# Kernel tuning notes

Measured on AMD Instinct MI355X. Metric: run time of the kernel, lower is better.

The kernel has to match this reference:

```python
import jax, jax.numpy as jnp
import numpy as np

B, N, H = 16384, 4, 768
HEADS, OUT = 4, H // 4
L = 3  # num_layers
NEG_SLOPE = 0.2
EPS = 1e-5


def layer_norm(x, g, b):
    m = jnp.mean(x, axis=-1, keepdims=True)
    v = jnp.mean((x - m) ** 2, axis=-1, keepdims=True)
    return (x - m) * jax.lax.rsqrt(v + EPS) * g + b


def setup_inputs() -> dict:
    key = jax.random.key(0)
    ks = jax.random.split(key, 12)
    s = 0.02
    return {
        "image_features": jax.random.normal(ks[0], (B, N, H), jnp.float32),
        "type_emb": s * jax.random.normal(ks[1], (N, H), jnp.float32),
        "W_gat": s * jax.random.normal(ks[2], (L, H, HEADS * OUT), jnp.float32),
        "att_src": s * jax.random.normal(ks[3], (L, HEADS, OUT), jnp.float32),
        "att_dst": s * jax.random.normal(ks[4], (L, HEADS, OUT), jnp.float32),
        "gat_bias": jnp.zeros((L, H), jnp.float32),
        "ln_gamma": jnp.ones((L, H), jnp.float32),
        "ln_beta": jnp.zeros((L, H), jnp.float32),
        "W1": s * jax.random.normal(ks[5], (L, H, 2 * H), jnp.float32),
        "b1": jnp.zeros((L, 2 * H), jnp.float32),
        "W2": s * jax.random.normal(ks[6], (L, 2 * H, H), jnp.float32),
        "b2": jnp.zeros((L, H), jnp.float32),
    }


def reference(image_features, type_emb, W_gat, att_src, att_dst, gat_bias,
              ln_gamma, ln_beta, W1, b1, W2, b2):
    # type embedding added per node type (N=4 fixed types)
    x = image_features + type_emb  # [B, N, H]
    for l in range(L):
        res = x
        # GATConv: fully-connected 4-node graph == dense per-head attention
        h = (x @ W_gat[l]).reshape(B, N, HEADS, OUT)          # [B, N, heads, out]
        a_s = jnp.einsum('bnhd,hd->bnh', h, att_src[l])        # alpha for source j
        a_d = jnp.einsum('bnhd,hd->bnh', h, att_dst[l])        # alpha for dest   i
        e = a_d[:, :, None, :] + a_s[:, None, :, :]            # [B, i, j, heads]
        e = jnp.where(e > 0, e, NEG_SLOPE * e)                 # leaky_relu(0.2)
        alpha = jax.nn.softmax(e, axis=2)                      # softmax over neighbors j
        out = jnp.einsum('bijh,bjhd->bihd', alpha, h).reshape(B, N, H) + gat_bias[l]
        x = layer_norm(out + res, ln_gamma[l], ln_beta[l])
        # FFN (dropout inactive at eval)
        ffn = jax.nn.relu(x @ W1[l] + b1[l]) @ W2[l] + b2[l]
        # NOTE: original module reuses the SAME LayerNorm for both residuals
        x = layer_norm(ffn + x, ln_gamma[l], ln_beta[l])
    return x
```

## Files before the change

kernel.cpp:

```cpp
#include <hip/hip_runtime.h>
#include <stdint.h>


typedef __bf16 bf16x8 __attribute__((ext_vector_type(8)));
typedef float  f32x4  __attribute__((ext_vector_type(4)));

__device__ __forceinline__ uint16_t f2bf(float f) {
  union { float f; uint32_t u; } v; v.f = f;
  uint32_t r = v.u + 0x7fffu + ((v.u >> 16) & 1u);
  return (uint16_t)(r >> 16);
}

__device__ __forceinline__ float wave_sum(float v) {
#pragma unroll
  for (int off = 32; off > 0; off >>= 1) v += __shfl_xor(v, off);
  return v;
}

__device__ __forceinline__ void gload_lds16(const void* g, void* l) {
  __builtin_amdgcn_global_load_lds(
      (const __attribute__((address_space(1))) void*)(g),
      (__attribute__((address_space(3))) void*)(l), 16, 0, 0);
}

template <int EPI>
__global__ __launch_bounds__(256, 2)
void gemm_bf16(const uint16_t* __restrict__ A, const uint16_t* __restrict__ Bt,
               const float* __restrict__ bias, void* __restrict__ Cv,
               int M, int N, int K) {
  __shared__ uint16_t As[128 * 32];
  __shared__ uint16_t Bs[128 * 32];

  int wgid = blockIdx.y * gridDim.x + blockIdx.x;
  const int nwg = gridDim.x * gridDim.y;
  if ((nwg & 7) == 0) wgid = (wgid & 7) * (nwg >> 3) + (wgid >> 3);
  const int bn = wgid % gridDim.x, bm = wgid / gridDim.x;

  const int t = threadIdx.x;
  const int w = t >> 6, lane = t & 63;
  const int wr = w >> 1, wc = w & 1;

  f32x4 acc[4][4] = {};

  const int srow = t >> 2;
  const int scol = (t & 3) * 8;
  const uint16_t* Ag = A  + (size_t)(bm * 128 + srow) * K + scol;
  const uint16_t* Bg = Bt + (size_t)(bn * 128 + srow) * K + scol;

  const int KT = K >> 5;
  for (int kt = 0; kt < KT; ++kt) {
    __syncthreads();
    gload_lds16(Ag,          &As[w * 512]);
    gload_lds16(Ag + 64 * K, &As[2048 + w * 512]);
    gload_lds16(Bg,          &Bs[w * 512]);
    gload_lds16(Bg + 64 * K, &Bs[2048 + w * 512]);
    Ag += 32; Bg += 32;
    asm volatile("s_waitcnt vmcnt(0)" ::: "memory");
    __syncthreads();

    const int fr = lane & 15;
    const int kg = (lane >> 4) * 8;
    bf16x8 a[4], b[4];
#pragma unroll
    for (int m = 0; m < 4; ++m)
      a[m] = *(const bf16x8*)&As[(wr * 64 + m * 16 + fr) * 32 + kg];
#pragma unroll
    for (int n = 0; n < 4; ++n)
      b[n] = *(const bf16x8*)&Bs[(wc * 64 + n * 16 + fr) * 32 + kg];
#pragma unroll
    for (int m = 0; m < 4; ++m)
#pragma unroll
      for (int n = 0; n < 4; ++n)
        acc[m][n] = __builtin_amdgcn_mfma_f32_16x16x32_bf16(a[m], b[n], acc[m][n], 0, 0, 0);
  }

  const int row0 = bm * 128 + wr * 64 + ((lane >> 4) * 4);
  const int col0 = bn * 128 + wc * 64 + (lane & 15);
#pragma unroll
  for (int m = 0; m < 4; ++m) {
#pragma unroll
    for (int n = 0; n < 4; ++n) {
      const int col = col0 + n * 16;
      const float bv = bias ? bias[col] : 0.0f;
#pragma unroll
      for (int j = 0; j < 4; ++j) {
        const int row = row0 + m * 16 + j;
        const float v = acc[m][n][j] + bv;
        if (EPI == 0) ((float*)Cv)[(size_t)row * N + col] = v;
        else ((uint16_t*)Cv)[(size_t)row * N + col] = f2bf(fmaxf(v, 0.0f));
      }
    }
  }
}

__global__ __launch_bounds__(256)
void transpose_f32_to_bf16(const float* __restrict__ W, uint16_t* __restrict__ Wt,
                           int R, int C) {
  __shared__ float tile[32][33];
  const size_t lofs = (size_t)blockIdx.z * R * C;
  W += lofs; Wt += lofs;
  const int c0 = blockIdx.x * 32, r0 = blockIdx.y * 32;
  const int t = threadIdx.x, tc = t & 31, tr = t >> 5;
#pragma unroll
  for (int i = 0; i < 4; ++i)
    tile[tr + i * 8][tc] = W[(size_t)(r0 + tr + i * 8) * C + c0 + tc];
  __syncthreads();
#pragma unroll
  for (int i = 0; i < 4; ++i)
    Wt[(size_t)(c0 + tr + i * 8) * R + r0 + tc] = f2bf(tile[tc][tr + i * 8]);
}

__global__ __launch_bounds__(256)
void init_x(const float* __restrict__ img, const float* __restrict__ te,
            float* __restrict__ xout, uint16_t* __restrict__ xb, int n4) {
  for (int i = blockIdx.x * 256 + threadIdx.x; i < n4; i += gridDim.x * 256) {
    const float4 a = ((const float4*)img)[i];
    const float4 b = ((const float4*)te)[i % 768];
    float4 o; o.x = a.x + b.x; o.y = a.y + b.y; o.z = a.z + b.z; o.w = a.w + b.w;
    ((float4*)xout)[i] = o;
    ushort4 p; p.x = f2bf(o.x); p.y = f2bf(o.y); p.z = f2bf(o.z); p.w = f2bf(o.w);
    ((ushort4*)xb)[i] = p;
  }
}

__global__ __launch_bounds__(256, 4)
void gat_attn_ln(const float* __restrict__ h, const float* __restrict__ xres,
                 const float* __restrict__ att_src, const float* __restrict__ att_dst,
                 const float* __restrict__ gbias, const float* __restrict__ gamma,
                 const float* __restrict__ beta, float* __restrict__ xout,
                 uint16_t* __restrict__ xb) {
  __shared__ float hs[4 * 768];
  __shared__ float as_[4][4], ad_[4][4];
  __shared__ float alpha[4][4][4];
  const int b = blockIdx.x;
  const int t = threadIdx.x, w = t >> 6, lane = t & 63;
  const size_t base = (size_t)b * 3072;

  {
    const float4* hg = (const float4*)(h + base);
    float4* hl = (float4*)hs;
    for (int i = t; i < 768; i += 256) hl[i] = hg[i];
  }
  __syncthreads();

  {
    const int n = w;
#pragma unroll
    for (int hd = 0; hd < 4; ++hd) {
      float ps = 0.f, pd = 0.f;
      for (int d = lane; d < 192; d += 64) {
        const float hv = hs[n * 768 + hd * 192 + d];
        ps += hv * att_src[hd * 192 + d];
        pd += hv * att_dst[hd * 192 + d];
      }
      ps = wave_sum(ps); pd = wave_sum(pd);
      if (lane == 0) { as_[n][hd] = ps; ad_[n][hd] = pd; }
    }
  }
  __syncthreads();

  if (t < 16) {
    const int i = t >> 2, hd = t & 3;
    float e[4], mx = -1e30f;
#pragma unroll
    for (int j = 0; j < 4; ++j) {
      float v = ad_[i][hd] + as_[j][hd];
      v = v > 0.f ? v : 0.2f * v;
      e[j] = v; mx = fmaxf(mx, v);
    }
    float s = 0.f;
#pragma unroll
    for (int j = 0; j < 4; ++j) { e[j] = __expf(e[j] - mx); s += e[j]; }
    const float inv = 1.0f / s;
#pragma unroll
    for (int j = 0; j < 4; ++j) alpha[i][hd][j] = e[j] * inv;
  }
  __syncthreads();

  const int i = w;
  float v[12];
  float mean = 0.f;
#pragma unroll
  for (int c0 = 0; c0 < 12; ++c0) {
    const int c = c0 * 64 + lane;
    const int hd = c / 192;
    float o = alpha[i][hd][0] * hs[c]        + alpha[i][hd][1] * hs[768 + c] +
              alpha[i][hd][2] * hs[1536 + c] + alpha[i][hd][3] * hs[2304 + c];
    o += gbias[c] + xres[base + i * 768 + c];
    v[c0] = o; mean += o;
  }
  mean = wave_sum(mean) * (1.0f / 768.0f);
  float var = 0.f;
#pragma unroll
  for (int c0 = 0; c0 < 12; ++c0) { const float d = v[c0] - mean; var += d * d; }
  var = wave_sum(var) * (1.0f / 768.0f);
  const float inv = rsqrtf(var + 1e-5f);
#pragma unroll
  for (int c0 = 0; c0 < 12; ++c0) {
    const int c = c0 * 64 + lane;
    const float y = (v[c0] - mean) * inv * gamma[c] + beta[c];
    const size_t idx = base + i * 768 + c;
    xout[idx] = y;
    xb[idx] = f2bf(y);
  }
}

__global__ __launch_bounds__(256, 4)
void ffn_ln(const float* __restrict__ ffn, const float* __restrict__ xres,
            const float* __restrict__ gamma, const float* __restrict__ beta,
            float* __restrict__ xout, uint16_t* __restrict__ xb, int write_xb) {
  const int t = threadIdx.x, w = t >> 6, lane = t & 63;
  const size_t row = (size_t)blockIdx.x * 4 + w;
  const size_t base = row * 768;
  const float4* fg = (const float4*)(ffn + base);
  const float4* xg = (const float4*)(xres + base);
  float4 v[3];
  float mean = 0.f;
#pragma unroll
  for (int k = 0; k < 3; ++k) {
    const int i = k * 64 + lane;
    const float4 a = fg[i], b = xg[i];
    v[k].x = a.x + b.x; v[k].y = a.y + b.y; v[k].z = a.z + b.z; v[k].w = a.w + b.w;
    mean += v[k].x + v[k].y + v[k].z + v[k].w;
  }
  mean = wave_sum(mean) * (1.0f / 768.0f);
  float var = 0.f;
#pragma unroll
  for (int k = 0; k < 3; ++k) {
    const float dx = v[k].x - mean, dy = v[k].y - mean;
    const float dz = v[k].z - mean, dw = v[k].w - mean;
    var += dx * dx + dy * dy + dz * dz + dw * dw;
  }
  var = wave_sum(var) * (1.0f / 768.0f);
  const float inv = rsqrtf(var + 1e-5f);
#pragma unroll
  for (int k = 0; k < 3; ++k) {
    const int i = k * 64 + lane;
    const float4 g = ((const float4*)gamma)[i], bb = ((const float4*)beta)[i];
    float4 y;
    y.x = (v[k].x - mean) * inv * g.x + bb.x;
    y.y = (v[k].y - mean) * inv * g.y + bb.y;
    y.z = (v[k].z - mean) * inv * g.z + bb.z;
    y.w = (v[k].w - mean) * inv * g.w + bb.w;
    ((float4*)(xout + base))[i] = y;
    if (write_xb) {
      ushort4 p; p.x = f2bf(y.x); p.y = f2bf(y.y); p.z = f2bf(y.z); p.w = f2bf(y.w);
      ((ushort4*)(xb + base))[i] = p;
    }
  }
}

extern "C" void kernel_launch(void* const* d_in, const int* in_sizes, int n_in,
                              void* d_out, int out_size, void* d_ws, size_t ws_size,
                              hipStream_t stream) {
  const float* img   = (const float*)d_in[0];
  const float* te    = (const float*)d_in[1];
  const float* Wgat  = (const float*)d_in[2];
  const float* asrc  = (const float*)d_in[3];
  const float* adst  = (const float*)d_in[4];
  const float* gbias = (const float*)d_in[5];
  const float* gam   = (const float*)d_in[6];
  const float* bet   = (const float*)d_in[7];
  const float* W1    = (const float*)d_in[8];
  const float* b1    = (const float*)d_in[9];
  const float* W2    = (const float*)d_in[10];
  const float* b2    = (const float*)d_in[11];

  const int B = 16384;
  const size_t ROWS = (size_t)B * 4;
  const size_t XE = ROWS * 768;

  float* g_f32 = (float*)d_out;

  uint8_t* p = (uint8_t*)d_ws;
  float*    x_f32 = (float*)p;    p += XE * 4;
  uint16_t* xb    = (uint16_t*)p; p += XE * 2;
  uint16_t* mid   = (uint16_t*)p; p += ROWS * 1536 * 2;
  uint16_t* wtg   = (uint16_t*)p; p += (size_t)3 * 768 * 768 * 2;
  uint16_t* wt1   = (uint16_t*)p; p += (size_t)3 * 1536 * 768 * 2;
  uint16_t* wt2   = (uint16_t*)p; p += (size_t)3 * 768 * 1536 * 2;

  transpose_f32_to_bf16<<<dim3(24, 24, 3), 256, 0, stream>>>(Wgat, wtg, 768, 768);
  transpose_f32_to_bf16<<<dim3(48, 24, 3), 256, 0, stream>>>(W1,   wt1, 768, 1536);
  transpose_f32_to_bf16<<<dim3(24, 48, 3), 256, 0, stream>>>(W2,   wt2, 1536, 768);
  init_x<<<2048, 256, 0, stream>>>(img, te, x_f32, xb, (int)(XE / 4));

  for (int l = 0; l < 3; ++l) {
    gemm_bf16<0><<<dim3(768 / 128, ROWS / 128), 256, 0, stream>>>(
        xb, wtg + (size_t)l * 768 * 768, nullptr, g_f32, (int)ROWS, 768, 768);
    gat_attn_ln<<<B, 256, 0, stream>>>(
        g_f32, x_f32, asrc + l * 768, adst + l * 768, gbias + l * 768,
        gam + l * 768, bet + l * 768, x_f32, xb);
    gemm_bf16<1><<<dim3(1536 / 128, ROWS / 128), 256, 0, stream>>>(
        xb, wt1 + (size_t)l * 1536 * 768, b1 + l * 1536, mid, (int)ROWS, 1536, 768);
    gemm_bf16<0><<<dim3(768 / 128, ROWS / 128), 256, 0, stream>>>(
        mid, wt2 + (size_t)l * 768 * 1536, b2 + l * 768, g_f32, (int)ROWS, 768, 1536);
    float* xo = (l == 2) ? (float*)d_out : x_f32;
    ffn_ln<<<ROWS / 4, 256, 0, stream>>>(
        g_f32, x_f32, gam + l * 768, bet + l * 768, xo, xb, (l == 2) ? 0 : 1);
  }
}
```

Measured before the change: 2.927 ms.

## Replace GEMM with 256x256 double-buffered, swizzled-LDS, 8-wave pipelined kernel

Replaces the 128x128 tile, single-buffered GEMM with a 256x256 tile kernel using 512 threads, 128KB dynamic LDS, and BK=64. Global-to-LDS loads for the next K-step are double-buffered and overlap with MFMA work. LDS uses an XOR swizzle to avoid bank conflicts. Compute is split into four quadrants separated by barriers and s_setprio, so the waves interleave loads and MFMAs. The larger tile increases data reuse per block, but with only one block per CU the grid is small (768/256 x 256 = 768 blocks), which risks tail effects and extra barrier overhead.

Result: faster. 2.716 ms (-7.2%).

```diff
diff --git a/kernel.cpp b/kernel.cpp
--- a/kernel.cpp
+++ b/kernel.cpp
@@ -24,68 +24,119 @@
 }
 
 template <int EPI>
-__global__ __launch_bounds__(256, 2)
-void gemm_bf16(const uint16_t* __restrict__ A, const uint16_t* __restrict__ Bt,
-               const float* __restrict__ bias, void* __restrict__ Cv,
-               int M, int N, int K) {
-  __shared__ uint16_t As[128 * 32];
-  __shared__ uint16_t Bs[128 * 32];
+__global__ __launch_bounds__(512, 1)
+void gemm256_bf16(const uint16_t* __restrict__ A, const uint16_t* __restrict__ Bt,
+                  const float* __restrict__ bias, void* __restrict__ Cv,
+                  int M, int N, int K) {
+  extern __shared__ uint16_t lds[];
 
   int wgid = blockIdx.y * gridDim.x + blockIdx.x;
   const int nwg = gridDim.x * gridDim.y;
-  if ((nwg & 7) == 0) wgid = (wgid & 7) * (nwg >> 3) + (wgid >> 3);
+  wgid = (wgid & 7) * (nwg >> 3) + (wgid >> 3);
   const int bn = wgid % gridDim.x, bm = wgid / gridDim.x;
 
   const int t = threadIdx.x;
   const int w = t >> 6, lane = t & 63;
-  const int wr = w >> 1, wc = w & 1;
-
-  f32x4 acc[4][4] = {};
-
-  const int srow = t >> 2;
-  const int scol = (t & 3) * 8;
-  const uint16_t* Ag = A  + (size_t)(bm * 128 + srow) * K + scol;
-  const uint16_t* Bg = Bt + (size_t)(bn * 128 + srow) * K + scol;
-
-  const int KT = K >> 5;
+  const int wm = w >> 2, wn = w & 3;
+  const int fr = lane & 15, kg = lane >> 4;
+  const int frx = fr & 7;
+  const int rl = lane >> 3;
+  const int sblk = (lane & 7) ^ rl;
+
+  const uint16_t* Ag = A  + (size_t)(bm * 256 + w * 8 + rl) * K + sblk * 8;
+  const uint16_t* Bg = Bt + (size_t)(bn * 256 + w * 8 + rl) * K + sblk * 8;
+
+  f32x4 acc[8][4] = {};
+  bf16x8 a[4][2], b[2][2];
+
+#define STAGE(CO, DA, DB)                                                     \
+  do {                                                                        \
+    _Pragma("unroll") for (int j = 0; j < 4; ++j) {                           \
+      gload_lds16(Ag + (size_t)(j * 64) * K + (CO), (DA) + (w * 8 + j * 64) * 64); \
+      gload_lds16(Bg + (size_t)(j * 64) * K + (CO), (DB) + (w * 8 + j * 64) * 64); \
+    }                                                                         \
+  } while (0)
+
+#define LOADA(MH)                                                             \
+  do {                                                                        \
+    _Pragma("unroll") for (int fm = 0; fm < 4; ++fm) {                        \
+      const int rowA = wm * 128 + (MH)*64 + fm * 16 + fr;                     \
+      a[fm][0] = *(const bf16x8*)&ldsA[rowA * 64 + ((kg) ^ frx) * 8];         \
+      a[fm][1] = *(const bf16x8*)&ldsA[rowA * 64 + ((4 + kg) ^ frx) * 8];     \
+    }                                                                         \
+  } while (0)
+
+#define LOADB(NH)                                                             \
+  do {                                                                        \
+    _Pragma("unroll") for (int fn = 0; fn < 2; ++fn) {                        \
+      const int rowB = wn * 64 + (NH)*32 + fn * 16 + fr;                      \
+      b[fn][0] = *(const bf16x8*)&ldsB[rowB * 64 + ((kg) ^ frx) * 8];         \
+      b[fn][1] = *(const bf16x8*)&ldsB[rowB * 64 + ((4 + kg) ^ frx) * 8];     \
+    }                                                                         \
+  } while (0)
+
+#define MFMA_Q(MH, NH)                                                        \
+  do {                                                                        \
+    _Pragma("unroll") for (int fm = 0; fm < 4; ++fm)                          \
+    _Pragma("unroll") for (int fn = 0; fn < 2; ++fn)                          \
+    _Pragma("unroll") for (int ks = 0; ks < 2; ++ks)                          \
+      acc[(MH)*4 + fm][(NH)*2 + fn] = __builtin_amdgcn_mfma_f32_16x16x32_bf16( \
+          a[fm][ks], b[fn][ks], acc[(MH)*4 + fm][(NH)*2 + fn], 0, 0, 0);      \
+  } while (0)
+
+#define BAR __builtin_amdgcn_s_barrier()
+#define PRIO1 __builtin_amdgcn_s_setprio(1)
+#define PRIO0 __builtin_amdgcn_s_setprio(0)
+
+  const int KT = K >> 6;
+
+  STAGE(0, lds, lds + 32768);
+  asm volatile("s_waitcnt vmcnt(0)" ::: "memory");
+  BAR;
+
   for (int kt = 0; kt < KT; ++kt) {
-    __syncthreads();
-    gload_lds16(Ag,          &As[w * 512]);
-    gload_lds16(Ag + 64 * K, &As[2048 + w * 512]);
-    gload_lds16(Bg,          &Bs[w * 512]);
-    gload_lds16(Bg + 64 * K, &Bs[2048 + w * 512]);
-    Ag += 32; Bg += 32;
-    asm volatile("s_waitcnt vmcnt(0)" ::: "memory");
-    __syncthreads();
-
-    const int fr = lane & 15;
-    const int kg = (lane >> 4) * 8;
-    bf16x8 a[4], b[4];
-#pragma unroll
-    for (int m = 0; m < 4; ++m)
-      a[m] = *(const bf16x8*)&As[(wr * 64 + m * 16 + fr) * 32 + kg];
-#pragma unroll
-    for (int n = 0; n < 4; ++n)
-      b[n] = *(const bf16x8*)&Bs[(wc * 64 + n * 16 + fr) * 32 + kg];
-#pragma unroll
-    for (int m = 0; m < 4; ++m)
-#pragma unroll
-      for (int n = 0; n < 4; ++n)
-        acc[m][n] = __builtin_amdgcn_mfma_f32_16x16x32_bf16(a[m], b[n], acc[m][n], 0, 0, 0);
-  }
-
-  const int row0 = bm * 128 + wr * 64 + ((lane >> 4) * 4);
-  const int col0 = bn * 128 + wc * 64 + (lane & 15);
-#pragma unroll
-  for (int m = 0; m < 4; ++m) {
-#pragma unroll
-    for (int n = 0; n < 4; ++n) {
-      const int col = col0 + n * 16;
+    const uint16_t* ldsA = lds + (kt & 1) * 16384;
+    const uint16_t* ldsB = lds + 32768 + (kt & 1) * 16384;
+    const bool st = (kt + 1 < KT);
+
+    LOADA(0);
+    LOADB(0);
+    if (st) {
+      uint16_t* dA = lds + ((kt + 1) & 1) * 16384;
+      uint16_t* dB = lds + 32768 + ((kt + 1) & 1) * 16384;
+      STAGE((size_t)(kt + 1) * 64, dA, dB);
+    }
+    BAR; PRIO1; MFMA_Q(0, 0); PRIO0; BAR;
+    LOADB(1);
+    BAR; PRIO1; MFMA_Q(0, 1); PRIO0; BAR;
+    LOADA(1);
+    BAR; PRIO1; MFMA_Q(1, 1); PRIO0; BAR;
+    LOADB(0);
+    BAR; PRIO1; MFMA_Q(1, 0); PRIO0;
+    if (st) asm volatile("s_waitcnt vmcnt(0)" ::: "memory");
+    BAR;
+  }
+
+#undef STAGE
+#undef LOADA
+#undef LOADB
+#undef MFMA_Q
+#undef BAR
+#undef PRIO1
+#undef PRIO0
+
+  const int row0 = bm * 256 + wm * 128 + (lane >> 4) * 4;
+  const int col0 = bn * 256 + wn * 64 + fr;
+#pragma unroll
+  for (int mf = 0; mf < 8; ++mf) {
+#pragma unroll
+    for (int nf = 0; nf < 4; ++nf) {
+      const int col = col0 + nf * 16;
       const float bv = bias ? bias[col] : 0.0f;
 #pragma unroll
-      for (int j = 0; j < 4; ++j) {
-        const int row = row0 + m * 16 + j;
-        const float v = acc[m][n][j] + bv;
+      for (int jj = 0; jj < 4; ++jj) {
+        const int row = row0 + mf * 16 + jj;
+        const float v = acc[mf][nf][jj] + bv;
         if (EPI == 0) ((float*)Cv)[(size_t)row * N + col] = v;
         else ((uint16_t*)Cv)[(size_t)row * N + col] = f2bf(fmaxf(v, 0.0f));
       }
@@ -270,6 +321,11 @@
   const size_t ROWS = (size_t)B * 4;
   const size_t XE = ROWS * 768;
 
+  (void)hipFuncSetAttribute(reinterpret_cast<const void*>(&gemm256_bf16<0>),
+                            hipFuncAttributeMaxDynamicSharedMemorySize, 131072);
+  (void)hipFuncSetAttribute(reinterpret_cast<const void*>(&gemm256_bf16<1>),
+                            hipFuncAttributeMaxDynamicSharedMemorySize, 131072);
+
   float* g_f32 = (float*)d_out;
 
   uint8_t* p = (uint8_t*)d_ws;
@@ -286,14 +342,14 @@
   init_x<<<2048, 256, 0, stream>>>(img, te, x_f32, xb, (int)(XE / 4));
 
   for (int l = 0; l < 3; ++l) {
-    gemm_bf16<0><<<dim3(768 / 128, ROWS / 128), 256, 0, stream>>>(
+    gemm256_bf16<0><<<dim3(768 / 256, ROWS / 256), 512, 131072, stream>>>(
         xb, wtg + (size_t)l * 768 * 768, nullptr, g_f32, (int)ROWS, 768, 768);
     gat_attn_ln<<<B, 256, 0, stream>>>(
         g_f32, x_f32, asrc + l * 768, adst + l * 768, gbias + l * 768,
         gam + l * 768, bet + l * 768, x_f32, xb);
-    gemm_bf16<1><<<dim3(1536 / 128, ROWS / 128), 256, 0, stream>>>(
+    gemm256_bf16<1><<<dim3(1536 / 256, ROWS / 256), 512, 131072, stream>>>(
         xb, wt1 + (size_t)l * 1536 * 768, b1 + l * 1536, mid, (int)ROWS, 1536, 768);
-    gemm_bf16<0><<<dim3(768 / 128, ROWS / 128), 256, 0, stream>>>(
+    gemm256_bf16<0><<<dim3(768 / 256, ROWS / 256), 512, 131072, stream>>>(
         mid, wt2 + (size_t)l * 768 * 1536, b2 + l * 768, g_f32, (int)ROWS, 768, 1536);
     float* xo = (l == 2) ? (float*)d_out : x_f32;
     ffn_ln<<<ROWS / 4, 256, 0, stream>>>(
```
